# Performance work log

Hardware: AMD Instinct MI355X
Metric: run time of the kernel (lower is better)

Reference implementation:

```python
import jax, jax.numpy as jnp
import numpy as np

N, DIM, HID, E = 100000, 128, 512, 600000


def setup_inputs() -> dict:
    key = jax.random.key(0)
    k_h, k_src, k_dst, k_w1, k_b1, k_w2, k_b2 = jax.random.split(key, 7)
    h = jax.random.normal(k_h, (N, DIM), dtype=jnp.float32)
    src = jax.random.randint(k_src, (E,), 0, N)
    dst = jax.random.randint(k_dst, (E,), 0, N)
    edge_index = jnp.stack([src, dst], axis=0).astype(jnp.int64)
    # Linear params stored as [in, out] (math-equivalent to torch's [out,in].T)
    s1 = 1.0 / np.sqrt(2 * DIM)
    s2 = 1.0 / np.sqrt(HID)
    W1 = jax.random.uniform(k_w1, (2 * DIM, HID), jnp.float32, -s1, s1)
    b1 = jax.random.uniform(k_b1, (HID,), jnp.float32, -s1, s1)
    W2 = jax.random.uniform(k_w2, (HID, DIM), jnp.float32, -s2, s2)
    b2 = jax.random.uniform(k_b2, (DIM,), jnp.float32, -s2, s2)
    return {"h": h, "edge_index": edge_index, "W1": W1, "b1": b1, "W2": W2, "b2": b2}


def reference(h, edge_index, W1, b1, W2, b2):
    src, dst = edge_index[0], edge_index[1]
    n = h.shape[0]
    # scatter-mean: sum gathered neighbor features per destination node
    agg_sum = jax.ops.segment_sum(h[src], dst, num_segments=n)  # [N, DIM]
    deg = jax.ops.segment_sum(jnp.ones((src.shape[0],), h.dtype), dst, num_segments=n)  # [N]
    mean = agg_sum / jnp.maximum(deg, 1.0)[:, None]
    # isolated nodes (deg==0) fall back to their own features
    agg = jnp.where((deg == 0)[:, None], h, mean)
    x = jnp.concatenate([h, agg], axis=-1)  # [N, 2*DIM]
    hdn = jax.nn.gelu(x @ W1 + b1, approximate=False)  # torch GELU default = exact erf
    return hdn @ W2 + b2
```

## Files before the change

### kernel.cpp

```cpp
#include <hip/hip_runtime.h>
#include <hip/hip_bf16.h>
#include <math.h>

#define N_NODES 100000
#define DIM 128
#define HID 512
#define EDGES 600000
#define SCAN_CHUNK 1024
#define SCAN_NBLK ((N_NODES + SCAN_CHUNK - 1) / SCAN_CHUNK)
#define MROWS_PAD 100096
#define NCH1 (MROWS_PAD / 64)
#define NCH2 (MROWS_PAD / 32)
#define GEMM_GRID 512

typedef short bf16x8 __attribute__((ext_vector_type(8)));
typedef float f32x4 __attribute__((ext_vector_type(4)));


__device__ inline unsigned short f32_to_bf16(float f) {
    unsigned int u = __float_as_uint(f);
    u += 0x7fff + ((u >> 16) & 1);
    return (unsigned short)(u >> 16);
}

__device__ inline float gelu_f(float x) {
    float x3 = x * x * x;
    float y = 0.7978845608028654f * x + 0.0356774081f * x3;
    float e = exp2f(y * 2.8853900817779268f);
    float t = 1.0f - 2.0f * __builtin_amdgcn_rcpf(e + 1.0f);
    return 0.5f * x * (1.0f + t);
}

__device__ inline void gload16(const void* g, void* l) {
    __builtin_amdgcn_global_load_lds(
        (const __attribute__((address_space(1))) unsigned int*)g,
        (__attribute__((address_space(3))) unsigned int*)l,
        16, 0, 0);
}

#define PREP_W1_BLKS 512
#define PREP_W2_BLKS 128
#define PREP_CONV_BLKS 12500
#define PREP_COUNT_BLKS ((EDGES + 255) / 256)
#define PREP_TOTAL (PREP_W1_BLKS + PREP_W2_BLKS + PREP_CONV_BLKS + PREP_COUNT_BLKS)

__global__ __launch_bounds__(256) void mgl_prep_kernel(
    const float* __restrict__ h, const int* __restrict__ ei,
    const float* __restrict__ W1, const float* __restrict__ W2,
    unsigned short* __restrict__ X, unsigned short* __restrict__ W1T,
    unsigned short* __restrict__ W2T, int* __restrict__ cnt)
{
    int b = blockIdx.x;
    if (b < PREP_W1_BLKS) {
        int n = b;
        int k = threadIdx.x;
        unsigned short val = f32_to_bf16(W1[(size_t)k * HID + n]);
        int byteoff = (k * 2) ^ ((n & 7) << 4);
        *(unsigned short*)((char*)(W1T + (size_t)n * 256) + byteoff) = val;
        return;
    }
    b -= PREP_W1_BLKS;
    if (b < PREP_W2_BLKS) {
        int n = b;
        #pragma unroll
        for (int it = 0; it < 2; ++it) {
            int k = threadIdx.x + it * 256;
            unsigned short val = f32_to_bf16(W2[(size_t)k * DIM + n]);
            int byteoff = (k * 2) ^ ((n & 7) << 4);
            *(unsigned short*)((char*)(W2T + (size_t)n * 512) + byteoff) = val;
        }
        return;
    }
    b -= PREP_W2_BLKS;
    if (b < PREP_CONV_BLKS) {
        int t = b * 256 + threadIdx.x;
        if (t >= N_NODES * (DIM / 4)) return;
        int node = t >> 5;
        int c4 = t & 31;
        float4 v = *(const float4*)(h + (size_t)node * DIM + c4 * 4);
        ushort4 p;
        p.x = f32_to_bf16(v.x); p.y = f32_to_bf16(v.y);
        p.z = f32_to_bf16(v.z); p.w = f32_to_bf16(v.w);
        int byteoff = (c4 * 8) ^ ((node & 7) << 4);
        *(ushort4*)((char*)(X + (size_t)node * 256) + byteoff) = p;
        return;
    }
    b -= PREP_CONV_BLKS;
    {
        int e = b * 256 + threadIdx.x;
        if (e < EDGES) atomicAdd(&cnt[ei[EDGES + e]], 1);
    }
}

__global__ __launch_bounds__(256) void mgl_scan_block_kernel(
    const int* __restrict__ cnt, int* __restrict__ row_start, int* __restrict__ bsum)
{
    __shared__ int sdata[256];
    int t = threadIdx.x;
    int base = blockIdx.x * SCAN_CHUNK + t * 4;
    int v[4];
    #pragma unroll
    for (int i = 0; i < 4; ++i) {
        int idx = base + i;
        v[i] = (idx < N_NODES) ? cnt[idx] : 0;
    }
    int tsum = v[0] + v[1] + v[2] + v[3];
    sdata[t] = tsum;
    __syncthreads();
    for (int off = 1; off < 256; off <<= 1) {
        int x = (t >= off) ? sdata[t - off] : 0;
        __syncthreads();
        sdata[t] += x;
        __syncthreads();
    }
    int run = (t > 0) ? sdata[t - 1] : 0;
    #pragma unroll
    for (int i = 0; i < 4; ++i) {
        int idx = base + i;
        if (idx < N_NODES) row_start[idx] = run;
        run += v[i];
    }
    if (t == 255) bsum[blockIdx.x] = sdata[255];
}

__global__ __launch_bounds__(128) void mgl_scan_bsum_kernel(int* __restrict__ bsum)
{
    __shared__ int sd[128];
    int t = threadIdx.x;
    int v = (t < SCAN_NBLK) ? bsum[t] : 0;
    sd[t] = v;
    __syncthreads();
    for (int off = 1; off < 128; off <<= 1) {
        int x = (t >= off) ? sd[t - off] : 0;
        __syncthreads();
        sd[t] += x;
        __syncthreads();
    }
    if (t < SCAN_NBLK) bsum[t] = sd[t] - v;
}

__global__ __launch_bounds__(256) void mgl_scan_add_kernel(
    int* __restrict__ row_start, const int* __restrict__ bsum)
{
    int i = blockIdx.x * 256 + threadIdx.x;
    if (i < N_NODES) row_start[i] += bsum[i / SCAN_CHUNK];
    if (i == 0) row_start[N_NODES] = EDGES;
}

__global__ __launch_bounds__(256) void mgl_fill_kernel(
    const int* __restrict__ ei, const int* __restrict__ row_start,
    int* __restrict__ cnt, int* __restrict__ csr)
{
    int e = blockIdx.x * 256 + threadIdx.x;
    if (e >= EDGES) return;
    int s = ei[e];
    int t = ei[EDGES + e];
    int pos = atomicSub(&cnt[t], 1) - 1;
    csr[row_start[t] + pos] = s;
}

__global__ __launch_bounds__(256) void mgl_gather_mean_kernel(
    const unsigned short* __restrict__ Xb, const int* __restrict__ row_start,
    const int* __restrict__ csr, unsigned short* __restrict__ X)
{
    int v = blockIdx.x * 4 + (threadIdx.x >> 6);
    if (v >= N_NODES) return;
    int lane = threadIdx.x & 63;
    int beg = row_start[v];
    int nb = row_start[v + 1] - beg;
    int laneByte = lane * 4;
    const char* xb = (const char*)Xb;

    if (nb > 0) {
        float2 acc = make_float2(0.f, 0.f);
        for (int base = 0; base < nb; base += 64) {
            int rem = nb - base; if (rem > 64) rem = 64;
            int sv = (lane < rem) ? csr[beg + base + lane] : 0;
            for (int j = 0; j < rem; ++j) {
                int s = __shfl(sv, j);
                unsigned int pk = *(const unsigned int*)(
                    xb + (size_t)s * 512 + (laneByte ^ ((s & 7) << 4)));
                acc.x += __uint_as_float(pk << 16);
                acc.y += __uint_as_float(pk & 0xffff0000u);
            }
        }
        float inv = 1.f / (float)nb;
        unsigned int po = (unsigned int)f32_to_bf16(acc.x * inv) |
                          ((unsigned int)f32_to_bf16(acc.y * inv) << 16);
        *(unsigned int*)((char*)(X + (size_t)v * 256) +
                         ((256 + laneByte) ^ ((v & 7) << 4))) = po;
    } else {
        unsigned int pk = *(const unsigned int*)(
            xb + (size_t)v * 512 + (laneByte ^ ((v & 7) << 4)));
        *(unsigned int*)((char*)(X + (size_t)v * 256) +
                         ((256 + laneByte) ^ ((v & 7) << 4))) = pk;
    }
}

__global__ __launch_bounds__(512, 2) void mgl_mlp1_kernel(
    const unsigned short* __restrict__ W1T,
    const unsigned short* __restrict__ Xr,
    const float* __restrict__ b1f,
    unsigned short* __restrict__ hdn)
{
    __shared__ char ldsX[2 * 32768];
    const int tid = threadIdx.x;
    const int w = tid >> 6, l = tid & 63;
    const int r16 = l & 15, kq = l >> 4;
    const int rmask = (r16 & 7) << 4;
    const int n0w = w * 64;

    bf16x8 a1[4][8];
    #pragma unroll
    for (int nb = 0; nb < 4; ++nb) {
        const char* wrow = (const char*)W1T + (size_t)(n0w + nb * 16 + r16) * 512;
        #pragma unroll
        for (int ks = 0; ks < 8; ++ks)
            a1[nb][ks] = *(const bf16x8*)(wrow + ((ks * 64 + kq * 16) ^ rmask));
    }
    float4 b1v[4];
    #pragma unroll
    for (int nb = 0; nb < 4; ++nb)
        b1v[nb] = *(const float4*)(b1f + n0w + nb * 16 + kq * 4);

    const int bid = blockIdx.x;
    const int nch = (NCH1 - bid + GEMM_GRID - 1) / GEMM_GRID;

    auto stage = [&](int slot, int cj) {
        const char* src = (const char*)Xr + (size_t)cj * 32768;
        char* dst = ldsX + slot * 32768;
        #pragma unroll
        for (int i = 0; i < 4; ++i) {
            int off = i * 8192 + tid * 16;
            gload16(src + off, dst + off);
        }
    };

    stage(0, bid);

    for (int j = 0; j < nch; ++j) {
        if (j == 0) asm volatile("s_waitcnt vmcnt(0)" ::: "memory");
        else        asm volatile("s_waitcnt vmcnt(16)" ::: "memory");
        __builtin_amdgcn_s_barrier();
        asm volatile("" ::: "memory");
        if (j + 1 < nch) stage((j + 1) & 1, bid + (j + 1) * GEMM_GRID);

        const char* bX = ldsX + (j & 1) * 32768;
        f32x4 acc[4][4] = {};
        #pragma unroll
        for (int ks = 0; ks < 8; ++ks) {
            bf16x8 b[4];
            #pragma unroll
            for (int mb = 0; mb < 4; ++mb)
                b[mb] = *(const bf16x8*)(bX + (mb * 16 + r16) * 512 +
                                         ((ks * 64 + kq * 16) ^ rmask));
            #pragma unroll
            for (int mb = 0; mb < 4; ++mb)
                #pragma unroll
                for (int nb = 0; nb < 4; ++nb)
                    acc[mb][nb] = __builtin_amdgcn_mfma_f32_16x16x32_bf16(
                        a1[nb][ks], b[mb], acc[mb][nb], 0, 0, 0);
        }

        const size_t m0c = (size_t)(bid + j * GEMM_GRID) * 64;
        #pragma unroll
        for (int mb = 0; mb < 4; ++mb) {
            size_t m = m0c + mb * 16 + r16;
            char* hrow = (char*)hdn + m * 1024;
            #pragma unroll
            for (int nb = 0; nb < 4; ++nb) {
                int nc = n0w + nb * 16 + kq * 4;
                ushort4 pk;
                pk.x = f32_to_bf16(gelu_f(acc[mb][nb][0] + b1v[nb].x));
                pk.y = f32_to_bf16(gelu_f(acc[mb][nb][1] + b1v[nb].y));
                pk.z = f32_to_bf16(gelu_f(acc[mb][nb][2] + b1v[nb].z));
                pk.w = f32_to_bf16(gelu_f(acc[mb][nb][3] + b1v[nb].w));
                *(ushort4*)(hrow + ((nc * 2) ^ rmask)) = pk;
            }
        }
    }
}

__global__ __launch_bounds__(512, 2) void mgl_mlp2_kernel(
    const unsigned short* __restrict__ W2T,
    const unsigned short* __restrict__ hdn,
    const float* __restrict__ b2f,
    float* __restrict__ outp)
{
    __shared__ char ldsH[2 * 32768];
    const int tid = threadIdx.x;
    const int w = tid >> 6, l = tid & 63;
    const int r16 = l & 15, kq = l >> 4;
    const int rmask = (r16 & 7) << 4;

    bf16x8 a2[16];
    {
        const char* wrow = (const char*)W2T + (size_t)(w * 16 + r16) * 1024;
        #pragma unroll
        for (int ks = 0; ks < 16; ++ks)
            a2[ks] = *(const bf16x8*)(wrow + ((ks * 64 + kq * 16) ^ rmask));
    }
    float4 b2v = *(const float4*)(b2f + w * 16 + kq * 4);

    const int bid = blockIdx.x;
    const int nch = (NCH2 - bid + GEMM_GRID - 1) / GEMM_GRID;

    auto stage = [&](int slot, int cj) {
        const char* src = (const char*)hdn + (size_t)cj * 32768;
        char* dst = ldsH + slot * 32768;
        #pragma unroll
        for (int i = 0; i < 4; ++i) {
            int off = i * 8192 + tid * 16;
            gload16(src + off, dst + off);
        }
    };

    stage(0, bid);

    for (int j = 0; j < nch; ++j) {
        if (j == 0) asm volatile("s_waitcnt vmcnt(0)" ::: "memory");
        else        asm volatile("s_waitcnt vmcnt(2)" ::: "memory");
        __builtin_amdgcn_s_barrier();
        asm volatile("" ::: "memory");
        if (j + 1 < nch) stage((j + 1) & 1, bid + (j + 1) * GEMM_GRID);

        const char* bH = ldsH + (j & 1) * 32768;
        f32x4 acc[2] = {};
        #pragma unroll
        for (int ks = 0; ks < 16; ++ks) {
            bf16x8 b[2];
            #pragma unroll
            for (int mb = 0; mb < 2; ++mb)
                b[mb] = *(const bf16x8*)(bH + (mb * 16 + r16) * 1024 +
                                         ((ks * 64 + kq * 16) ^ rmask));
            #pragma unroll
            for (int mb = 0; mb < 2; ++mb)
                acc[mb] = __builtin_amdgcn_mfma_f32_16x16x32_bf16(
                    a2[ks], b[mb], acc[mb], 0, 0, 0);
        }

        const size_t m0c = (size_t)(bid + j * GEMM_GRID) * 32;
        #pragma unroll
        for (int mb = 0; mb < 2; ++mb) {
            size_t m = m0c + mb * 16 + r16;
            if (m < N_NODES) {
                float4 o;
                o.x = acc[mb][0] + b2v.x;
                o.y = acc[mb][1] + b2v.y;
                o.z = acc[mb][2] + b2v.z;
                o.w = acc[mb][3] + b2v.w;
                *(float4*)(outp + m * DIM + w * 16 + kq * 4) = o;
            }
        }
    }
}

extern "C" void kernel_launch(void* const* d_in, const int* in_sizes, int n_in,
                              void* d_out, int out_size, void* d_ws, size_t ws_size,
                              hipStream_t stream) {
    const float* h  = (const float*)d_in[0];
    const int*   ei = (const int*)d_in[1];
    const float* W1 = (const float*)d_in[2];
    const float* b1 = (const float*)d_in[3];
    const float* W2 = (const float*)d_in[4];
    const float* b2 = (const float*)d_in[5];
    float* out = (float*)d_out;

    unsigned short* X   = (unsigned short*)d_ws;
    unsigned short* hdn = X + (size_t)MROWS_PAD * 256;
    unsigned short* W1T = hdn + (size_t)MROWS_PAD * 512;
    unsigned short* W2T = W1T + 512 * 256;
    int* cnt = (int*)(W2T + 128 * 512);
    int* row_start = cnt + N_NODES;
    int* bsum = row_start + N_NODES + 1;
    int* csr = bsum + 128;

    hipMemsetAsync(cnt, 0, N_NODES * sizeof(int), stream);
    mgl_prep_kernel<<<PREP_TOTAL, 256, 0, stream>>>(h, ei, W1, W2, X, W1T, W2T, cnt);
    mgl_scan_block_kernel<<<SCAN_NBLK, 256, 0, stream>>>(cnt, row_start, bsum);
    mgl_scan_bsum_kernel<<<1, 128, 0, stream>>>(bsum);
    mgl_scan_add_kernel<<<(N_NODES + 255) / 256, 256, 0, stream>>>(row_start, bsum);
    mgl_fill_kernel<<<(EDGES + 255) / 256, 256, 0, stream>>>(ei, row_start, cnt, csr);
    mgl_gather_mean_kernel<<<(N_NODES + 3) / 4, 256, 0, stream>>>(X, row_start, csr, X);

    mgl_mlp1_kernel<<<GEMM_GRID, 512, 0, stream>>>(W1T, X, b1, hdn);
    mgl_mlp2_kernel<<<GEMM_GRID, 512, 0, stream>>>(W2T, hdn, b2, out);
}
```

Baseline: 234.0 us.

## Split MLP1 hidden dimension across block pairs and raise occupancy to four blocks

MLP1 now assigns each block half of the 512 hidden columns, so each wave holds 2 N-blocks of W1 in registers instead of 4. That halves the weight and accumulator register footprint, which allows launch bounds of 4 blocks per CU for both GEMM kernels. The cost is that each X chunk is now staged from global memory by two blocks instead of one. The MFMA inner loops are also reordered to load one B fragment per step, and the wait count is adjusted to match.

```diff
diff --git a/kernel.cpp b/kernel.cpp
--- a/kernel.cpp
+++ b/kernel.cpp
@@ -11,7 +11,6 @@
 #define MROWS_PAD 100096
 #define NCH1 (MROWS_PAD / 64)
 #define NCH2 (MROWS_PAD / 32)
-#define GEMM_GRID 512
 
 typedef short bf16x8 __attribute__((ext_vector_type(8)));
 typedef float f32x4 __attribute__((ext_vector_type(4)));
@@ -197,7 +196,7 @@
     }
 }
 
-__global__ __launch_bounds__(512, 2) void mgl_mlp1_kernel(
+__global__ __launch_bounds__(512, 4) void mgl_mlp1_kernel(
     const unsigned short* __restrict__ W1T,
     const unsigned short* __restrict__ Xr,
     const float* __restrict__ b1f,
@@ -208,23 +207,24 @@
     const int w = tid >> 6, l = tid & 63;
     const int r16 = l & 15, kq = l >> 4;
     const int rmask = (r16 & 7) << 4;
-    const int n0w = w * 64;
-
-    bf16x8 a1[4][8];
+    const int half = blockIdx.x & 1;
+    const int ms = blockIdx.x >> 1;
+    const int nbase = half * 256 + w * 32;
+
+    bf16x8 a1[2][8];
     #pragma unroll
-    for (int nb = 0; nb < 4; ++nb) {
-        const char* wrow = (const char*)W1T + (size_t)(n0w + nb * 16 + r16) * 512;
+    for (int nb = 0; nb < 2; ++nb) {
+        const char* wrow = (const char*)W1T + (size_t)(nbase + nb * 16 + r16) * 512;
         #pragma unroll
         for (int ks = 0; ks < 8; ++ks)
             a1[nb][ks] = *(const bf16x8*)(wrow + ((ks * 64 + kq * 16) ^ rmask));
     }
-    float4 b1v[4];
+    float4 b1v[2];
     #pragma unroll
-    for (int nb = 0; nb < 4; ++nb)
-        b1v[nb] = *(const float4*)(b1f + n0w + nb * 16 + kq * 4);
-
-    const int bid = blockIdx.x;
-    const int nch = (NCH1 - bid + GEMM_GRID - 1) / GEMM_GRID;
+    for (int nb = 0; nb < 2; ++nb)
+        b1v[nb] = *(const float4*)(b1f + nbase + nb * 16 + kq * 4);
+
+    const int nch = (NCH1 - ms + 255) >> 8;
 
     auto stage = [&](int slot, int cj) {
         const char* src = (const char*)Xr + (size_t)cj * 32768;
@@ -236,40 +236,37 @@
         }
     };
 
-    stage(0, bid);
+    stage(0, ms);
 
     for (int j = 0; j < nch; ++j) {
         if (j == 0) asm volatile("s_waitcnt vmcnt(0)" ::: "memory");
-        else        asm volatile("s_waitcnt vmcnt(16)" ::: "memory");
+        else        asm volatile("s_waitcnt vmcnt(8)" ::: "memory");
         __builtin_amdgcn_s_barrier();
-        asm volatile("" ::: "memory");
-        if (j + 1 < nch) stage((j + 1) & 1, bid + (j + 1) * GEMM_GRID);
+        if (j + 1 < nch) stage((j + 1) & 1, ms + (j + 1) * 256);
 
         const char* bX = ldsX + (j & 1) * 32768;
-        f32x4 acc[4][4] = {};
+        f32x4 acc[4][2] = {};
         #pragma unroll
         for (int ks = 0; ks < 8; ++ks) {
-            bf16x8 b[4];
             #pragma unroll
-            for (int mb = 0; mb < 4; ++mb)
-                b[mb] = *(const bf16x8*)(bX + (mb * 16 + r16) * 512 +
-                                         ((ks * 64 + kq * 16) ^ rmask));
-            #pragma unroll
-            for (int mb = 0; mb < 4; ++mb)
-                #pragma unroll
-                for (int nb = 0; nb < 4; ++nb)
-                    acc[mb][nb] = __builtin_amdgcn_mfma_f32_16x16x32_bf16(
-                        a1[nb][ks], b[mb], acc[mb][nb], 0, 0, 0);
-        }
-
-        const size_t m0c = (size_t)(bid + j * GEMM_GRID) * 64;
+            for (int mb = 0; mb < 4; ++mb) {
+                bf16x8 b = *(const bf16x8*)(bX + (mb * 16 + r16) * 512 +
+                                            ((ks * 64 + kq * 16) ^ rmask));
+                acc[mb][0] = __builtin_amdgcn_mfma_f32_16x16x32_bf16(
+                    a1[0][ks], b, acc[mb][0], 0, 0, 0);
+                acc[mb][1] = __builtin_amdgcn_mfma_f32_16x16x32_bf16(
+                    a1[1][ks], b, acc[mb][1], 0, 0, 0);
+            }
+        }
+
+        const size_t m0c = (size_t)(ms + j * 256) * 64;
         #pragma unroll
         for (int mb = 0; mb < 4; ++mb) {
             size_t m = m0c + mb * 16 + r16;
             char* hrow = (char*)hdn + m * 1024;
             #pragma unroll
-            for (int nb = 0; nb < 4; ++nb) {
-                int nc = n0w + nb * 16 + kq * 4;
+            for (int nb = 0; nb < 2; ++nb) {
+                int nc = nbase + nb * 16 + kq * 4;
                 ushort4 pk;
                 pk.x = f32_to_bf16(gelu_f(acc[mb][nb][0] + b1v[nb].x));
                 pk.y = f32_to_bf16(gelu_f(acc[mb][nb][1] + b1v[nb].y));
@@ -281,7 +278,7 @@
     }
 }
 
-__global__ __launch_bounds__(512, 2) void mgl_mlp2_kernel(
+__global__ __launch_bounds__(512, 4) void mgl_mlp2_kernel(
     const unsigned short* __restrict__ W2T,
     const unsigned short* __restrict__ hdn,
     const float* __restrict__ b2f,
@@ -303,7 +300,7 @@
     float4 b2v = *(const float4*)(b2f + w * 16 + kq * 4);
 
     const int bid = blockIdx.x;
-    const int nch = (NCH2 - bid + GEMM_GRID - 1) / GEMM_GRID;
+    const int nch = (NCH2 - bid + 511) >> 9;
 
     auto stage = [&](int slot, int cj) {
         const char* src = (const char*)hdn + (size_t)cj * 32768;
@@ -321,25 +318,22 @@
         if (j == 0) asm volatile("s_waitcnt vmcnt(0)" ::: "memory");
         else        asm volatile("s_waitcnt vmcnt(2)" ::: "memory");
         __builtin_amdgcn_s_barrier();
-        asm volatile("" ::: "memory");
-        if (j + 1 < nch) stage((j + 1) & 1, bid + (j + 1) * GEMM_GRID);
+        if (j + 1 < nch) stage((j + 1) & 1, bid + (j + 1) * 512);
 
         const char* bH = ldsH + (j & 1) * 32768;
         f32x4 acc[2] = {};
         #pragma unroll
         for (int ks = 0; ks < 16; ++ks) {
-            bf16x8 b[2];
             #pragma unroll
-            for (int mb = 0; mb < 2; ++mb)
-                b[mb] = *(const bf16x8*)(bH + (mb * 16 + r16) * 1024 +
-                                         ((ks * 64 + kq * 16) ^ rmask));
-            #pragma unroll
-            for (int mb = 0; mb < 2; ++mb)
+            for (int mb = 0; mb < 2; ++mb) {
+                bf16x8 b = *(const bf16x8*)(bH + (mb * 16 + r16) * 1024 +
+                                            ((ks * 64 + kq * 16) ^ rmask));
                 acc[mb] = __builtin_amdgcn_mfma_f32_16x16x32_bf16(
-                    a2[ks], b[mb], acc[mb], 0, 0, 0);
-        }
-
-        const size_t m0c = (size_t)(bid + j * GEMM_GRID) * 32;
+                    a2[ks], b, acc[mb], 0, 0, 0);
+            }
+        }
+
+        const size_t m0c = (size_t)(bid + j * 512) * 32;
         #pragma unroll
         for (int mb = 0; mb < 2; ++mb) {
             size_t m = m0c + mb * 16 + r16;
@@ -383,6 +377,6 @@
     mgl_fill_kernel<<<(EDGES + 255) / 256, 256, 0, stream>>>(ei, row_start, cnt, csr);
     mgl_gather_mean_kernel<<<(N_NODES + 3) / 4, 256, 0, stream>>>(X, row_start, csr, X);
 
-    mgl_mlp1_kernel<<<GEMM_GRID, 512, 0, stream>>>(W1T, X, b1, hdn);
-    mgl_mlp2_kernel<<<GEMM_GRID, 512, 0, stream>>>(W2T, hdn, b2, out);
-}
+    mgl_mlp1_kernel<<<512, 512, 0, stream>>>(W1T, X, b1, hdn);
+    mgl_mlp2_kernel<<<512, 512, 0, stream>>>(W2T, hdn, b2, out);
+}
```

Result: no change. 237.8 us (+1.6%).
